# Performance work log

Hardware: AMD Instinct MI355X
Metric: run time of the kernel (lower is better)

Reference implementation:

```python
import jax, jax.numpy as jnp
import numpy as np

NUM_SPINS = 1024
BATCH = 4096
INPUT_DIM = 2
NUM_HIDDEN = 128
NUM_LAYERS = 1
FIXED_MAG = 0


def setup_inputs() -> dict:
    key = jax.random.key(0)
    ks = jax.random.split(key, 7)
    # spins one-hot encoded, as the module's masking math assumes
    spins = jax.random.randint(ks[0], (NUM_SPINS, BATCH), 0, 2)
    data_in = jax.nn.one_hot(spins, INPUT_DIM, dtype=jnp.float32)
    s = 1.0 / np.sqrt(NUM_HIDDEN)  # torch RNNCell default uniform bound
    W_ih = jax.random.uniform(ks[1], (NUM_HIDDEN, INPUT_DIM), minval=-s, maxval=s, dtype=jnp.float32)
    W_hh = jax.random.uniform(ks[2], (NUM_HIDDEN, NUM_HIDDEN), minval=-s, maxval=s, dtype=jnp.float32)
    b_ih = jax.random.uniform(ks[3], (NUM_HIDDEN,), minval=-s, maxval=s, dtype=jnp.float32)
    b_hh = jax.random.uniform(ks[4], (NUM_HIDDEN,), minval=-s, maxval=s, dtype=jnp.float32)
    W_lin = jax.random.uniform(ks[5], (INPUT_DIM, NUM_HIDDEN), minval=-s, maxval=s, dtype=jnp.float32)
    b_lin = jax.random.uniform(ks[6], (INPUT_DIM,), minval=-s, maxval=s, dtype=jnp.float32)
    return {"data_in": data_in, "W_ih": W_ih, "W_hh": W_hh,
            "b_ih": b_ih, "b_hh": b_hh, "W_lin": W_lin, "b_lin": b_lin}


def reference(data_in, W_ih, W_hh, b_ih, b_hh, W_lin, b_lin):
    S, B, I = data_in.shape
    dt = data_in.dtype
    # input sequence shifted by one spin, first input is init_state [1,0]
    init_state = jnp.array([1.0, 0.0], dtype=dt)
    data = jnp.concatenate([jnp.broadcast_to(init_state, (1, B, I)), data_in[:-1]], axis=0)

    def step(h, x):
        for _ in range(NUM_LAYERS):  # source re-applies the SAME cell num_layers times
            h = jnp.tanh(x @ W_ih.T + b_ih + h @ W_hh.T + b_hh)
        probs = jax.nn.softmax(h @ W_lin.T + b_lin, axis=-1)
        return h, probs

    h0 = jnp.zeros((B, NUM_HIDDEN), dtype=dt)
    _, state_probs = jax.lax.scan(step, h0, data)  # [S, B, I]

    # conditional masking from fixed magnetization
    half = S // 2
    thresh_up = half + (S % 2) + FIXED_MAG // 2
    thresh_down = half - FIXED_MAG // 2
    cum_up = jnp.cumsum(data_in[:, :, 0], axis=0)    # [S, B]
    cum_down = jnp.cumsum(data_in[:, :, 1], axis=0)  # [S, B]
    down_guar = jnp.array([0.0, 1.0], dtype=dt)
    up_guar = jnp.array([1.0, 0.0], dtype=dt)
    mask_up = (cum_up[:-1] >= thresh_up)[..., None]      # for spins 1..S-1
    mask_down = (cum_down[:-1] >= thresh_down)[..., None]
    corr = jnp.where(mask_up, down_guar, state_probs[1:])
    corr = jnp.where(mask_down, up_guar, corr)
    return jnp.concatenate([state_probs[:1], corr], axis=0)
```

## Files before the change

kernel.cpp:

```cpp
#include <hip/hip_runtime.h>

#define NS 1024
#define NB 4096
#define NH 128
#define RB 16
#define NT 512

typedef __attribute__((ext_vector_type(8))) short short8;
typedef __attribute__((ext_vector_type(4))) float f32x4;

__device__ __forceinline__ short f2bf(float x) {
    unsigned u = __builtin_bit_cast(unsigned, x);
    u = (u + 0x7FFFu + ((u >> 16) & 1u)) >> 16;
    return (short)u;
}
__device__ __forceinline__ float vexp2(float x) {
    float r;
    asm("v_exp_f32 %0, %1" : "=v"(r) : "v"(x));
    return r;
}

#define BARRIER() asm volatile("s_waitcnt lgkmcnt(0)\n\ts_barrier" ::: "memory")

__global__ __launch_bounds__(NT, 1)
void pwf_kernel(const float* __restrict__ data_in,
                const float* __restrict__ W_ih,
                const float* __restrict__ W_hh,
                const float* __restrict__ b_ih,
                const float* __restrict__ b_hh,
                const float* __restrict__ W_lin,
                const float* __restrict__ b_lin,
                float* __restrict__ out)
{
    __shared__ __align__(16) short hlds[2][RB * NH];
    __shared__ unsigned selm[2];
    __shared__ uint2    msk[4];

    const int tid = threadIdx.x;
    const int w   = tid >> 6;
    const int l   = tid & 63;
    const int g   = l >> 4;
    const int b   = l & 15;
    const int b0  = blockIdx.x * RB;

    const float TL2E = 2.8853900817779268f;
    const float L2E  = 1.4426950408889634f;

    const int hrow = w * 16 + b;
    short8 afrag[4];
    #pragma unroll
    for (int kb = 0; kb < 4; ++kb) {
        const float* src = W_hh + hrow * NH + kb * 32 + g * 8;
        short8 v;
        #pragma unroll
        for (int i = 0; i < 8; ++i) v[i] = f2bf(TL2E * src[i]);
        afrag[kb] = v;
    }
    short8 lfrag[4];
    #pragma unroll
    for (int kb = 0; kb < 4; ++kb) {
        short8 v;
        #pragma unroll
        for (int i = 0; i < 8; ++i) {
            const int k = kb * 32 + g * 8 + i;
            v[i] = (b == 0) ? f2bf(L2E * (W_lin[NH + k] - W_lin[k])) : (short)0;
        }
        lfrag[kb] = v;
    }

    float cv0[4], cv1[4];
    #pragma unroll
    for (int r = 0; r < 4; ++r) {
        const int hid = w * 16 + 4 * g + r;
        const float cb = b_ih[hid] + b_hh[hid];
        cv0[r] = TL2E * (W_ih[hid * 2 + 0] + cb);
        cv1[r] = TL2E * (W_ih[hid * 2 + 1] + cb);
    }
    const float blD = L2E * (b_lin[1] - b_lin[0]);

    int aoff[4];
    #pragma unroll
    for (int kb = 0; kb < 4; ++kb)
        aoff[kb] = b * NH + ((kb * 32 + g * 8 + 8 * b) & 127);
    const int woffs = b * NH + ((w * 16 + 4 * g + 8 * b) & 127);

    ((uint4*)hlds)[tid] = make_uint4(0u, 0u, 0u, 0u);
    if (tid == 0) { selm[0] = 0u; msk[0] = make_uint2(0u, 0u); }
    int cntup = 0, cntdn = 0;
    const int rr = (l < RB) ? l : (RB - 1);
    float suA = 0.0f, suB = 0.0f;
    if (w == 7) {
        suA = data_in[(size_t)(b0 + rr) * 2];
        suB = data_in[((size_t)NB + b0 + rr) * 2];
    }
    float ediff = 0.0f;
    unsigned eum = 0u, edm = 0u;
    BARRIER();

#define STEP(T, P, SU)                                                         \
    {                                                                          \
        const short* hr = hlds[P];                                             \
        short* hw = hlds[(P) ^ 1];                                             \
        const unsigned sel = selm[P];                                          \
        const short8 h0 = *(const short8*)&hr[aoff[0]];                        \
        const short8 h1 = *(const short8*)&hr[aoff[1]];                        \
        const short8 h2 = *(const short8*)&hr[aoff[2]];                        \
        const short8 h3 = *(const short8*)&hr[aoff[3]];                        \
        if (w == 0 && (T) >= 2 && l < 16) {       \
            float p0 = __builtin_amdgcn_rcpf(1.0f + vexp2(ediff));             \
            float p1 = 1.0f - p0;                                              \
            if ((eum >> l) & 1u) { p0 = 0.0f; p1 = 1.0f; }                     \
            if ((edm >> l) & 1u) { p0 = 1.0f; p1 = 0.0f; }                     \
            *(float2*)&out[((size_t)((T) - 2) * NB + b0 + l) * 2] =            \
                make_float2(p0, p1);                                           \
        }                                                                      \
                           \
        f32x4 zz = {0.f, 0.f, 0.f, 0.f};                                       \
        f32x4 c01 = __builtin_amdgcn_mfma_f32_16x16x32_bf16(afrag[0], h0, zz, 0, 0, 0); \
        c01 = __builtin_amdgcn_mfma_f32_16x16x32_bf16(afrag[1], h1, c01, 0, 0, 0); \
        f32x4 c23 = __builtin_amdgcn_mfma_f32_16x16x32_bf16(afrag[2], h2, zz, 0, 0, 0); \
        c23 = __builtin_amdgcn_mfma_f32_16x16x32_bf16(afrag[3], h3, c23, 0, 0, 0); \
        if (w == 0 && (T) >= 1) {                \
            f32x4 d01 = __builtin_amdgcn_mfma_f32_16x16x32_bf16(lfrag[0], h0, zz, 0, 0, 0); \
            d01 = __builtin_amdgcn_mfma_f32_16x16x32_bf16(lfrag[1], h1, d01, 0, 0, 0); \
            f32x4 d23 = __builtin_amdgcn_mfma_f32_16x16x32_bf16(lfrag[2], h2, zz, 0, 0, 0); \
            d23 = __builtin_amdgcn_mfma_f32_16x16x32_bf16(lfrag[3], h3, d23, 0, 0, 0); \
            ediff = d01[0] + d23[0] + blD;     \
            const uint2 mm = msk[((T) - 1) & 3];                               \
            eum = mm.x; edm = mm.y;                                            \
        }                                                                      \
        const unsigned sb = (sel >> b) & 1u;                                   \
        float hn[4];                                                           \
        _Pragma("unroll")                                                      \
        for (int r = 0; r < 4; ++r) {                                          \
            const float cv = sb ? cv1[r] : cv0[r];                             \
            const float e  = vexp2(c01[r] + c23[r] + cv);                      \
            hn[r] = fmaf(__builtin_amdgcn_rcpf(e + 1.0f), -2.0f, 1.0f);        \
        }                                                                      \
        unsigned pk01, pk23;                                                   \
        asm("v_cvt_pk_bf16_f32 %0, %1, %2" : "=v"(pk01) : "v"(hn[0]), "v"(hn[1])); \
        asm("v_cvt_pk_bf16_f32 %0, %1, %2" : "=v"(pk23) : "v"(hn[2]), "v"(hn[3])); \
        *(uint2*)&hw[woffs] = make_uint2(pk01, pk23);    \
        if (w == 7) {         \
            const int isup = ((SU) > 0.5f) ? 1 : 0;                            \
            cntup += isup; cntdn += 1 - isup;                                  \
            const unsigned long long bs = __ballot(l < RB && isup == 0);       \
            const unsigned long long bu = __ballot(l < RB && cntup >= NS / 2); \
            const unsigned long long bd = __ballot(l < RB && cntdn >= NS / 2); \
            if (l == 0) {                                                      \
                selm[(P) ^ 1] = (unsigned)bs & 0xFFFFu;                        \
                msk[((T) + 1) & 3] =                                           \
                    make_uint2((unsigned)bu & 0xFFFFu, (unsigned)bd & 0xFFFFu);\
            }                                                                  \
            const int tn = ((T) + 2 < NS) ? (T) + 2 : NS - 1;                  \
            (SU) = data_in[((size_t)tn * NB + b0 + rr) * 2];                   \
        }                                                                      \
        BARRIER();                                                             \
    }

    for (int t = 0; t < NS; t += 2) {
        STEP(t, 0, suA)
        STEP(t + 1, 1, suB)
    }

    if (w == 0) {
        if (l < 16) {
            float p0 = __builtin_amdgcn_rcpf(1.0f + vexp2(ediff));
            float p1 = 1.0f - p0;
            if ((eum >> l) & 1u) { p0 = 0.0f; p1 = 1.0f; }
            if ((edm >> l) & 1u) { p0 = 1.0f; p1 = 0.0f; }
            *(float2*)&out[((size_t)(NS - 2) * NB + b0 + l) * 2] =
                make_float2(p0, p1);
        }
        const short* hr = hlds[0];
        const short8 h0 = *(const short8*)&hr[aoff[0]];
        const short8 h1 = *(const short8*)&hr[aoff[1]];
        const short8 h2 = *(const short8*)&hr[aoff[2]];
        const short8 h3 = *(const short8*)&hr[aoff[3]];
        f32x4 zz = {0.f, 0.f, 0.f, 0.f};
        f32x4 d01 = __builtin_amdgcn_mfma_f32_16x16x32_bf16(lfrag[0], h0, zz, 0, 0, 0);
        d01 = __builtin_amdgcn_mfma_f32_16x16x32_bf16(lfrag[1], h1, d01, 0, 0, 0);
        f32x4 d23 = __builtin_amdgcn_mfma_f32_16x16x32_bf16(lfrag[2], h2, zz, 0, 0, 0);
        d23 = __builtin_amdgcn_mfma_f32_16x16x32_bf16(lfrag[3], h3, d23, 0, 0, 0);
        const float fdiff = d01[0] + d23[0] + blD;
        const uint2 mm = msk[(NS - 1) & 3];
        if (l < 16) {
            float p0 = __builtin_amdgcn_rcpf(1.0f + vexp2(fdiff));
            float p1 = 1.0f - p0;
            if ((mm.x >> l) & 1u) { p0 = 0.0f; p1 = 1.0f; }
            if ((mm.y >> l) & 1u) { p0 = 1.0f; p1 = 0.0f; }
            *(float2*)&out[((size_t)(NS - 1) * NB + b0 + l) * 2] =
                make_float2(p0, p1);
        }
    }
}

extern "C" void kernel_launch(void* const* d_in, const int* in_sizes, int n_in,
                              void* d_out, int out_size, void* d_ws, size_t ws_size,
                              hipStream_t stream) {
    const float* data_in = (const float*)d_in[0];
    const float* W_ih    = (const float*)d_in[1];
    const float* W_hh    = (const float*)d_in[2];
    const float* b_ih    = (const float*)d_in[3];
    const float* b_hh    = (const float*)d_in[4];
    const float* W_lin   = (const float*)d_in[5];
    const float* b_lin   = (const float*)d_in[6];
    float* out = (float*)d_out;

    dim3 grid(NB / RB);
    dim3 block(NT);
    pwf_kernel<<<grid, block, 0, stream>>>(data_in, W_ih, W_hh, b_ih, b_hh,
                                           W_lin, b_lin, out);
}
```

Baseline: 415.5 us.

## Split output head across waves and compute spin masks per-thread without ballots

Removes the shared selm/msk bitmasks that wave 7 produced with ballots; every thread now tracks its own column's spin counters and input selector in registers, prefetching spins four steps ahead. The W_lin projection, which one wave used to compute with four serial MFMAs, is split across waves 0-3 (one MFMA each), with partial sums stored in LDS. A rotating wave among 4-7 then finishes the softmax and writes the output. This shortens the serial critical path on wave 0 inside each barrier-bounded step, at the cost of redundant per-thread counting and extra LDS traffic.

Result: slower. 436.4 us (+5.0%).

```diff
diff --git a/kernel.cpp b/kernel.cpp
--- a/kernel.cpp
+++ b/kernel.cpp
@@ -3,7 +3,7 @@
 #define NS 1024
 #define NB 4096
 #define NH 128
-#define RB 16
+#define HLF 512
 #define NT 512
 
 typedef __attribute__((ext_vector_type(8))) short short8;
@@ -21,6 +21,7 @@
 }
 
 #define BARRIER() asm volatile("s_waitcnt lgkmcnt(0)\n\ts_barrier" ::: "memory")
+#define MFMA __builtin_amdgcn_mfma_f32_16x16x32_bf16
 
 __global__ __launch_bounds__(NT, 1)
 void pwf_kernel(const float* __restrict__ data_in,
@@ -32,42 +33,41 @@
                 const float* __restrict__ b_lin,
                 float* __restrict__ out)
 {
-    __shared__ __align__(16) short hlds[2][RB * NH];
-    __shared__ unsigned selm[2];
-    __shared__ uint2    msk[4];
+    __shared__ __align__(16) short hlds[2][16 * NH];
+    __shared__ __align__(16) float lp[2][16][4];
 
     const int tid = threadIdx.x;
     const int w   = tid >> 6;
     const int l   = tid & 63;
     const int g   = l >> 4;
     const int b   = l & 15;
-    const int b0  = blockIdx.x * RB;
+    const int b0  = blockIdx.x * 16;
+    const int bb  = b0 + b;
+    const int ws  = w & 3;
 
     const float TL2E = 2.8853900817779268f;
     const float L2E  = 1.4426950408889634f;
 
     const int hrow = w * 16 + b;
-    short8 afrag[4];
+    short8 af0, af1, af2, af3;
+    {
+        short8 t[4];
+        #pragma unroll
+        for (int kb = 0; kb < 4; ++kb) {
+            const float* src = W_hh + hrow * NH + kb * 32 + g * 8;
+            short8 v;
+            #pragma unroll
+            for (int i = 0; i < 8; ++i) v[i] = f2bf(TL2E * src[i]);
+            t[kb] = v;
+        }
+        af0 = t[0]; af1 = t[1]; af2 = t[2]; af3 = t[3];
+    }
+    short8 lfrag;
     #pragma unroll
-    for (int kb = 0; kb < 4; ++kb) {
-        const float* src = W_hh + hrow * NH + kb * 32 + g * 8;
-        short8 v;
-        #pragma unroll
-        for (int i = 0; i < 8; ++i) v[i] = f2bf(TL2E * src[i]);
-        afrag[kb] = v;
-    }
-    short8 lfrag[4];
-    #pragma unroll
-    for (int kb = 0; kb < 4; ++kb) {
-        short8 v;
-        #pragma unroll
-        for (int i = 0; i < 8; ++i) {
-            const int k = kb * 32 + g * 8 + i;
-            v[i] = (b == 0) ? f2bf(L2E * (W_lin[NH + k] - W_lin[k])) : (short)0;
-        }
-        lfrag[kb] = v;
-    }
-
+    for (int i = 0; i < 8; ++i) {
+        const int k = 32 * ws + 8 * g + i;
+        lfrag[i] = (b == 0) ? f2bf(L2E * (W_lin[NH + k] - W_lin[k])) : (short)0;
+    }
     float cv0[4], cv1[4];
     #pragma unroll
     for (int r = 0; r < 4; ++r) {
@@ -82,115 +82,104 @@
     #pragma unroll
     for (int kb = 0; kb < 4; ++kb)
         aoff[kb] = b * NH + ((kb * 32 + g * 8 + 8 * b) & 127);
+    const int aoffP = b * NH + ((32 * ws + 8 * g + 8 * b) & 127);
     const int woffs = b * NH + ((w * 16 + 4 * g + 8 * b) & 127);
 
     ((uint4*)hlds)[tid] = make_uint4(0u, 0u, 0u, 0u);
-    if (tid == 0) { selm[0] = 0u; msk[0] = make_uint2(0u, 0u); }
-    int cntup = 0, cntdn = 0;
-    const int rr = (l < RB) ? l : (RB - 1);
-    float suA = 0.0f, suB = 0.0f;
-    if (w == 7) {
-        suA = data_in[(size_t)(b0 + rr) * 2];
-        suB = data_in[((size_t)NB + b0 + rr) * 2];
-    }
-    float ediff = 0.0f;
-    unsigned eum = 0u, edm = 0u;
+    int   cntup = 0, cntdn = 0, sel = 0;
+    int   e1u = 0, e1d = 0, e2u = 0, e2d = 0;
+    float s0 = data_in[((size_t)0 * NB + bb) * 2];
+    float s1 = data_in[((size_t)1 * NB + bb) * 2];
+    float s2 = data_in[((size_t)2 * NB + bb) * 2];
+    float s3 = data_in[((size_t)3 * NB + bb) * 2];
     BARRIER();
 
-#define STEP(T, P, SU)                                                         \
+#define STEP(T, P, PH, SU)                                                     \
     {                                                                          \
         const short* hr = hlds[P];                                             \
         short* hw = hlds[(P) ^ 1];                                             \
-        const unsigned sel = selm[P];                                          \
         const short8 h0 = *(const short8*)&hr[aoff[0]];                        \
         const short8 h1 = *(const short8*)&hr[aoff[1]];                        \
         const short8 h2 = *(const short8*)&hr[aoff[2]];                        \
         const short8 h3 = *(const short8*)&hr[aoff[3]];                        \
-        if (w == 0 && (T) >= 2 && l < 16) {       \
-            float p0 = __builtin_amdgcn_rcpf(1.0f + vexp2(ediff));             \
-            float p1 = 1.0f - p0;                                              \
-            if ((eum >> l) & 1u) { p0 = 0.0f; p1 = 1.0f; }                     \
-            if ((edm >> l) & 1u) { p0 = 1.0f; p1 = 0.0f; }                     \
-            *(float2*)&out[((size_t)((T) - 2) * NB + b0 + l) * 2] =            \
-                make_float2(p0, p1);                                           \
+        if (w == 4 + (PH)) {                 \
+            if ((T) >= 2 && l < 16) {                                          \
+                const float4 v = *(const float4*)&lp[(P) ^ 1][l][0];           \
+                const float d = v.x + v.y + v.z + v.w + blD;                   \
+                float p0 = __builtin_amdgcn_rcpf(1.0f + vexp2(d));             \
+                float p1 = 1.0f - p0;                                          \
+                if (e2u) { p0 = 0.0f; p1 = 1.0f; }                             \
+                if (e2d) { p0 = 1.0f; p1 = 0.0f; }         \
+                *(float2*)&out[((size_t)((T) - 2) * NB + b0 + l) * 2] =        \
+                    make_float2(p0, p1);                                       \
+            }                                                                  \
+        }                                                                      \
+        if (w < 4) {                      \
+            const short8 hp = *(const short8*)&hr[aoffP];                      \
+            f32x4 zl = {0.f, 0.f, 0.f, 0.f};                                   \
+            const f32x4 cl = MFMA(lfrag, hp, zl, 0, 0, 0);                     \
+            if (l < 16) lp[P][l][ws] = cl[0];                                  \
         }                                                                      \
                            \
         f32x4 zz = {0.f, 0.f, 0.f, 0.f};                                       \
-        f32x4 c01 = __builtin_amdgcn_mfma_f32_16x16x32_bf16(afrag[0], h0, zz, 0, 0, 0); \
-        c01 = __builtin_amdgcn_mfma_f32_16x16x32_bf16(afrag[1], h1, c01, 0, 0, 0); \
-        f32x4 c23 = __builtin_amdgcn_mfma_f32_16x16x32_bf16(afrag[2], h2, zz, 0, 0, 0); \
-        c23 = __builtin_amdgcn_mfma_f32_16x16x32_bf16(afrag[3], h3, c23, 0, 0, 0); \
-        if (w == 0 && (T) >= 1) {                \
-            f32x4 d01 = __builtin_amdgcn_mfma_f32_16x16x32_bf16(lfrag[0], h0, zz, 0, 0, 0); \
-            d01 = __builtin_amdgcn_mfma_f32_16x16x32_bf16(lfrag[1], h1, d01, 0, 0, 0); \
-            f32x4 d23 = __builtin_amdgcn_mfma_f32_16x16x32_bf16(lfrag[2], h2, zz, 0, 0, 0); \
-            d23 = __builtin_amdgcn_mfma_f32_16x16x32_bf16(lfrag[3], h3, d23, 0, 0, 0); \
-            ediff = d01[0] + d23[0] + blD;     \
-            const uint2 mm = msk[((T) - 1) & 3];                               \
-            eum = mm.x; edm = mm.y;                                            \
-        }                                                                      \
-        const unsigned sb = (sel >> b) & 1u;                                   \
+        f32x4 c01 = MFMA(af0, h0, zz, 0, 0, 0);                                \
+        c01 = MFMA(af1, h1, c01, 0, 0, 0);                                     \
+        f32x4 c23 = MFMA(af2, h2, zz, 0, 0, 0);                                \
+        c23 = MFMA(af3, h3, c23, 0, 0, 0);                                     \
+        e2u = e1u; e2d = e1d;                         \
+        e1u = (cntup >= HLF); e1d = (cntdn >= HLF);               \
         float hn[4];                                                           \
         _Pragma("unroll")                                                      \
         for (int r = 0; r < 4; ++r) {                                          \
-            const float cv = sb ? cv1[r] : cv0[r];                             \
+            const float cv = sel ? cv1[r] : cv0[r];                            \
             const float e  = vexp2(c01[r] + c23[r] + cv);                      \
             hn[r] = fmaf(__builtin_amdgcn_rcpf(e + 1.0f), -2.0f, 1.0f);        \
         }                                                                      \
         unsigned pk01, pk23;                                                   \
         asm("v_cvt_pk_bf16_f32 %0, %1, %2" : "=v"(pk01) : "v"(hn[0]), "v"(hn[1])); \
         asm("v_cvt_pk_bf16_f32 %0, %1, %2" : "=v"(pk23) : "v"(hn[2]), "v"(hn[3])); \
-        *(uint2*)&hw[woffs] = make_uint2(pk01, pk23);    \
-        if (w == 7) {         \
+        *(uint2*)&hw[woffs] = make_uint2(pk01, pk23);                          \
+        {                               \
             const int isup = ((SU) > 0.5f) ? 1 : 0;                            \
-            cntup += isup; cntdn += 1 - isup;                                  \
-            const unsigned long long bs = __ballot(l < RB && isup == 0);       \
-            const unsigned long long bu = __ballot(l < RB && cntup >= NS / 2); \
-            const unsigned long long bd = __ballot(l < RB && cntdn >= NS / 2); \
-            if (l == 0) {                                                      \
-                selm[(P) ^ 1] = (unsigned)bs & 0xFFFFu;                        \
-                msk[((T) + 1) & 3] =                                           \
-                    make_uint2((unsigned)bu & 0xFFFFu, (unsigned)bd & 0xFFFFu);\
-            }                                                                  \
-            const int tn = ((T) + 2 < NS) ? (T) + 2 : NS - 1;                  \
-            (SU) = data_in[((size_t)tn * NB + b0 + rr) * 2];                   \
+            cntup += isup; cntdn += 1 - isup; sel = 1 - isup;                  \
+            const int tn = ((T) + 4 < NS) ? (T) + 4 : NS - 1;                  \
+            (SU) = data_in[((size_t)tn * NB + bb) * 2];                        \
         }                                                                      \
         BARRIER();                                                             \
     }
 
-    for (int t = 0; t < NS; t += 2) {
-        STEP(t, 0, suA)
-        STEP(t + 1, 1, suB)
-    }
-
-    if (w == 0) {
-        if (l < 16) {
-            float p0 = __builtin_amdgcn_rcpf(1.0f + vexp2(ediff));
+    for (int t = 0; t < NS; t += 4) {
+        STEP(t,     0, 0, s0)
+        STEP(t + 1, 1, 1, s1)
+        STEP(t + 2, 0, 2, s2)
+        STEP(t + 3, 1, 3, s3)
+    }
+
+    if (w < 4) {
+        const short8 hp = *(const short8*)&hlds[0][aoffP];
+        f32x4 zl = {0.f, 0.f, 0.f, 0.f};
+        const f32x4 cl = MFMA(lfrag, hp, zl, 0, 0, 0);
+        if (l < 16) lp[0][l][ws] = cl[0];
+    }
+    BARRIER();
+    if (w == 4 && l < 16) {
+        {
+            const float4 v = *(const float4*)&lp[1][l][0];
+            const float d = v.x + v.y + v.z + v.w + blD;
+            float p0 = __builtin_amdgcn_rcpf(1.0f + vexp2(d));
             float p1 = 1.0f - p0;
-            if ((eum >> l) & 1u) { p0 = 0.0f; p1 = 1.0f; }
-            if ((edm >> l) & 1u) { p0 = 1.0f; p1 = 0.0f; }
-            *(float2*)&out[((size_t)(NS - 2) * NB + b0 + l) * 2] =
-                make_float2(p0, p1);
+            if (e2u) { p0 = 0.0f; p1 = 1.0f; }
+            if (e2d) { p0 = 1.0f; p1 = 0.0f; }
+            *(float2*)&out[((size_t)(NS - 2) * NB + b0 + l) * 2] = make_float2(p0, p1);
         }
-        const short* hr = hlds[0];
-        const short8 h0 = *(const short8*)&hr[aoff[0]];
-        const short8 h1 = *(const short8*)&hr[aoff[1]];
-        const short8 h2 = *(const short8*)&hr[aoff[2]];
-        const short8 h3 = *(const short8*)&hr[aoff[3]];
-        f32x4 zz = {0.f, 0.f, 0.f, 0.f};
-        f32x4 d01 = __builtin_amdgcn_mfma_f32_16x16x32_bf16(lfrag[0], h0, zz, 0, 0, 0);
-        d01 = __builtin_amdgcn_mfma_f32_16x16x32_bf16(lfrag[1], h1, d01, 0, 0, 0);
-        f32x4 d23 = __builtin_amdgcn_mfma_f32_16x16x32_bf16(lfrag[2], h2, zz, 0, 0, 0);
-        d23 = __builtin_amdgcn_mfma_f32_16x16x32_bf16(lfrag[3], h3, d23, 0, 0, 0);
-        const float fdiff = d01[0] + d23[0] + blD;
-        const uint2 mm = msk[(NS - 1) & 3];
-        if (l < 16) {
-            float p0 = __builtin_amdgcn_rcpf(1.0f + vexp2(fdiff));
+        {
+            const float4 v = *(const float4*)&lp[0][l][0];
+            const float d = v.x + v.y + v.z + v.w + blD;
+            float p0 = __builtin_amdgcn_rcpf(1.0f + vexp2(d));
             float p1 = 1.0f - p0;
-            if ((mm.x >> l) & 1u) { p0 = 0.0f; p1 = 1.0f; }
-            if ((mm.y >> l) & 1u) { p0 = 1.0f; p1 = 0.0f; }
-            *(float2*)&out[((size_t)(NS - 1) * NB + b0 + l) * 2] =
-                make_float2(p0, p1);
+            if (e1u) { p0 = 0.0f; p1 = 1.0f; }
+            if (e1d) { p0 = 1.0f; p1 = 0.0f; }
+            *(float2*)&out[((size_t)(NS - 1) * NB + b0 + l) * 2] = make_float2(p0, p1);
         }
     }
 }
@@ -207,7 +196,7 @@
     const float* b_lin   = (const float*)d_in[6];
     float* out = (float*)d_out;
 
-    dim3 grid(NB / RB);
+    dim3 grid(NB / 16);
     dim3 block(NT);
     pwf_kernel<<<grid, block, 0, stream>>>(data_in, W_ih, W_hh, b_ih, b_hh,
                                            W_lin, b_lin, out);
```
